# Performance work log

Measured on AMD Instinct MI355X. Metric: run time of the kernel, lower is better.

## Reference

```python
import jax, jax.numpy as jnp
import numpy as np

B, T, D, H = 4, 1024, 1024, 16
DH = D // H
BETA = 0.9


def setup_inputs() -> dict:
    key = jax.random.key(0)
    ks = jax.random.split(key, 9)
    s = 1.0 / np.sqrt(D)
    return {
        "x": jax.random.normal(ks[0], (B, T, D), jnp.float32),
        "l3_memory": jax.random.normal(ks[1], (B, 1, D), jnp.float32),
        "wq": jax.random.normal(ks[2], (D, D), jnp.float32) * s,
        "wk": jax.random.normal(ks[3], (D, D), jnp.float32) * s,
        "wv": jax.random.normal(ks[4], (D, D), jnp.float32) * s,
        "wo": jax.random.normal(ks[5], (D, D), jnp.float32) * s,
        "rw1": jax.random.normal(ks[6], (D, D // 2), jnp.float32) * s,
        "rb1": jnp.zeros((D // 2,), jnp.float32),
        "rw2": jax.random.normal(ks[7], (D // 2, 3), jnp.float32) * (1.0 / np.sqrt(D // 2)),
        "rb2": jnp.zeros((3,), jnp.float32),
    }


def reference(x, l3_memory, wq, wk, wv, wo, rw1, rb1, rw2, rb2):
    b, t, d = x.shape
    dh = d // H

    def heads(y):  # [b,t,d] -> [b,h,t,dh]
        return y.reshape(b, t, H, dh).transpose(0, 2, 1, 3)

    q = x @ wq
    qh = heads(q)

    # L2: causal prefix EMA along time: y_t = beta*y_{t-1} + (1-beta)*x_t, y_{-1}=0
    def ema_step(c, xt):
        y = BETA * c + (1.0 - BETA) * xt
        return y, y
    _, l2 = jax.lax.scan(ema_step, jnp.zeros((b, d), x.dtype), jnp.swapaxes(x, 0, 1))
    l2 = jnp.swapaxes(l2, 0, 1)

    # L3: retrieval memory repeated to sequence length
    l3 = jnp.broadcast_to(l3_memory, (b, t, d))

    mask = jnp.tril(jnp.ones((t, t), bool))
    neg = jnp.finfo(x.dtype).min
    scale = 1.0 / np.sqrt(dh)

    def attend(mem):
        kh = heads(mem @ wk)
        vh = heads(mem @ wv)
        s = jnp.einsum('bhqd,bhkd->bhqk', qh, kh) * scale
        s = jnp.where(mask[None, None], s, neg)
        p = jax.nn.softmax(s, axis=-1)
        return jnp.einsum('bhqk,bhkd->bhqd', p, vh)

    # router over q tokens -> softmax mixture weights [b,t,3]
    hdn = jax.nn.gelu(q @ rw1 + rb1, approximate=False)
    lam = jax.nn.softmax(hdn @ rw2 + rb2, axis=-1)

    mixed = jnp.zeros((b, H, t, dh), x.dtype)
    for i, mem in enumerate((x, l2, l3)):
        mixed = mixed + lam[:, None, :, i:i + 1] * attend(mem)

    out = mixed.transpose(0, 2, 1, 3).reshape(b, t, d) @ wo
    return out, lam
```

## Files before the change

kernel.cpp:

```cpp
#include <hip/hip_runtime.h>
#include <hip/hip_bf16.h>
#include <math.h>


#define B_ 4
#define T_ 1024
#define D_ 1024
#define H_ 16
#define DH_ 64
#define M_ 4096

#define ECH 64
#define NCH 16

typedef __attribute__((ext_vector_type(8))) short bf16x8;
typedef __attribute__((ext_vector_type(4))) short s16x4;
typedef __attribute__((ext_vector_type(4))) float f32x4;

__device__ inline short f2b(float f) {
  __hip_bfloat16 h = __float2bfloat16(f);
  return *reinterpret_cast<short*>(&h);
}

__device__ inline void gload_lds16(const short* g, short* l) {
  __builtin_amdgcn_global_load_lds(
      (const __attribute__((address_space(1))) unsigned int*)g,
      (__attribute__((address_space(3))) unsigned int*)l, 16, 0, 0);
}

__global__ __launch_bounds__(256) void ema_chunk_kernel(const float* __restrict__ x,
                                                        float* __restrict__ l2,
                                                        short* __restrict__ xb) {
  int idx = blockIdx.x * 256 + threadIdx.x;
  int d = idx & (D_ - 1);
  int ch = (idx >> 10) & (NCH - 1);
  int b = idx >> 14;
  const float* xp = x + (size_t)(b * T_ + ch * ECH) * D_ + d;
  float* yp = l2 + (size_t)(b * T_ + ch * ECH) * D_ + d;
  short* xbp = xb + (size_t)(b * T_ + ch * ECH) * D_ + d;
  float y = 0.f;
#pragma unroll 4
  for (int t = 0; t < ECH; ++t) {
    float xv = xp[t * D_];
    y = 0.9f * y + 0.1f * xv;
    yp[t * D_] = y;
    xbp[t * D_] = f2b(xv);
  }
}

__global__ __launch_bounds__(256) void ema_carry_kernel(const float* __restrict__ l2,
                                                        float* __restrict__ g) {
  int idx = blockIdx.x * 256 + threadIdx.x;
  int d = idx & (D_ - 1);
  int b = idx >> 10;
  const float b64 = 0.0011790184577739f;
  float G = 0.f;
  for (int ch = 0; ch < NCH; ++ch) {
    g[(size_t)(b * NCH + ch) * D_ + d] = G;
    float lf = l2[(size_t)(b * T_ + ch * ECH + ECH - 1) * D_ + d];
    G = lf + b64 * G;
  }
}

__global__ __launch_bounds__(256) void ema_fix_kernel(const float* __restrict__ l2,
                                                      const float* __restrict__ g,
                                                      short* __restrict__ l2b) {
  int idx = blockIdx.x * 256 + threadIdx.x;
  int d = idx & (D_ - 1);
  int t = (idx >> 10) & (T_ - 1);
  int b = idx >> 20;
  int ch = t >> 6;
  int off = t & (ECH - 1);
  float G = g[(size_t)(b * NCH + ch) * D_ + d];
  float p9 = exp2f((float)(off + 1) * -0.15200309344504997f);
  l2b[idx] = f2b(l2[idx] + p9 * G);
}

__global__ __launch_bounds__(256) void transpose_w_kernel(
    const float* __restrict__ w0, const float* __restrict__ w1,
    const float* __restrict__ w2, const float* __restrict__ w3,
    const float* __restrict__ w4,
    short* __restrict__ t0, short* __restrict__ t1, short* __restrict__ t2,
    short* __restrict__ t3, short* __restrict__ t4) {
  int z = blockIdx.z;
  const float* W = (z == 0) ? w0 : (z == 1) ? w1 : (z == 2) ? w2 : (z == 3) ? w3 : w4;
  short* Wt = (z == 0) ? t0 : (z == 1) ? t1 : (z == 2) ? t2 : (z == 3) ? t3 : t4;
  int cols = (z == 4) ? 512 : 1024;
  int c0 = blockIdx.x * 32, r0 = blockIdx.y * 32;
  if (c0 >= cols) return;
  __shared__ float tile[32][33];
  int tc = threadIdx.x & 31, tr8 = threadIdx.x >> 5;
#pragma unroll
  for (int i = 0; i < 4; ++i)
    tile[tr8 + i * 8][tc] = W[(size_t)(r0 + tr8 + i * 8) * cols + c0 + tc];
  __syncthreads();
#pragma unroll
  for (int i = 0; i < 4; ++i) {
    int rr = tr8 + i * 8;
    Wt[(size_t)(c0 + rr) * 1024 + r0 + tc] = f2b(tile[tc][rr]);
  }
}

template <int NB>
__global__ __launch_bounds__(256) void gemm_bt(const short* __restrict__ A, int lda,
                                               const short* __restrict__ Bt,
                                               float* __restrict__ Cf,
                                               short* __restrict__ Cb,
                                               int Ndim, int Kdim) {
  __shared__ short As[128 * 64];
  __shared__ short Bs[NB * 64];
  constexpr int NW = NB / 64;
  constexpr int NF = 4;
  constexpr int MF = (NW == 2) ? 4 : 2;
  int tid = threadIdx.x;
  int w = tid >> 6, l = tid & 63;
  int lg = l >> 4, ll = l & 15;
  int wr = (NW == 2) ? (w >> 1) : w;
  int wc = (NW == 2) ? (w & 1) : 0;
  int row0 = blockIdx.y * 128, col0 = blockIdx.x * NB;

  f32x4 acc[MF][NF];
#pragma unroll
  for (int m = 0; m < MF; ++m)
#pragma unroll
    for (int n = 0; n < NF; ++n) acc[m][n] = (f32x4){0.f, 0.f, 0.f, 0.f};

  for (int k0 = 0; k0 < Kdim; k0 += 64) {
    __syncthreads();
#pragma unroll
    for (int it = 0; it < 4; ++it) {
      int s = it * 256 + w * 64 + l;
      int r = s >> 3;
      int c = (s & 7) ^ (r & 7);
      gload_lds16(A + (size_t)(row0 + r) * lda + k0 + c * 8, &As[(it * 256 + w * 64) * 8]);
    }
#pragma unroll
    for (int it = 0; it < NB / 32; ++it) {
      int s = it * 256 + w * 64 + l;
      int r = s >> 3;
      int c = (s & 7) ^ (r & 7);
      gload_lds16(Bt + (size_t)(col0 + r) * Kdim + k0 + c * 8, &Bs[(it * 256 + w * 64) * 8]);
    }
    __syncthreads();
#pragma unroll
    for (int ks = 0; ks < 2; ++ks) {
      bf16x8 af[MF], bfr[NF];
#pragma unroll
      for (int m = 0; m < MF; ++m) {
        int r = wr * (MF * 16) + m * 16 + ll;
        af[m] = *(const bf16x8*)&As[r * 64 + (((ks * 4 + lg) ^ (r & 7)) << 3)];
      }
#pragma unroll
      for (int n = 0; n < NF; ++n) {
        int r = wc * 64 + n * 16 + ll;
        bfr[n] = *(const bf16x8*)&Bs[r * 64 + (((ks * 4 + lg) ^ (r & 7)) << 3)];
      }
#pragma unroll
      for (int m = 0; m < MF; ++m)
#pragma unroll
        for (int n = 0; n < NF; ++n)
          acc[m][n] = __builtin_amdgcn_mfma_f32_16x16x32_bf16(af[m], bfr[n], acc[m][n], 0, 0, 0);
    }
  }
#pragma unroll
  for (int m = 0; m < MF; ++m) {
    int gr = row0 + wr * (MF * 16) + m * 16 + lg * 4;
#pragma unroll
    for (int n = 0; n < NF; ++n) {
      int gc = col0 + wc * 64 + n * 16 + ll;
#pragma unroll
      for (int r = 0; r < 4; ++r) {
        float vv = acc[m][n][r];
        if (Cf) Cf[(size_t)(gr + r) * Ndim + gc] = vv;
        if (Cb) Cb[(size_t)(gr + r) * Ndim + gc] = f2b(vv);
      }
    }
  }
}

__global__ __launch_bounds__(256) void gemm_dual(const short* __restrict__ xb,
                                                 const short* __restrict__ l2b,
                                                 const short* __restrict__ wqkvT,
                                                 short* __restrict__ QKV,
                                                 short* __restrict__ KV2) {
  const short* A;
  const short* Bt;
  short* Cb;
  int Ndim, col0;
  int bx = blockIdx.x;
  if (bx < 24) {
    A = xb; Bt = wqkvT; Cb = QKV; Ndim = 3072; col0 = bx * 128;
  } else {
    A = l2b; Bt = wqkvT + 1024 * 1024; Cb = KV2; Ndim = 2048; col0 = (bx - 24) * 128;
  }
  __shared__ short As[128 * 64];
  __shared__ short Bs[128 * 64];
  int tid = threadIdx.x;
  int w = tid >> 6, l = tid & 63;
  int lg = l >> 4, ll = l & 15;
  int wr = w >> 1, wc = w & 1;
  int row0 = blockIdx.y * 128;

  f32x4 acc[4][4];
#pragma unroll
  for (int m = 0; m < 4; ++m)
#pragma unroll
    for (int n = 0; n < 4; ++n) acc[m][n] = (f32x4){0.f, 0.f, 0.f, 0.f};

  for (int k0 = 0; k0 < 1024; k0 += 64) {
    __syncthreads();
#pragma unroll
    for (int it = 0; it < 4; ++it) {
      int s = it * 256 + w * 64 + l;
      int r = s >> 3;
      int c = (s & 7) ^ (r & 7);
      gload_lds16(A + (size_t)(row0 + r) * 1024 + k0 + c * 8, &As[(it * 256 + w * 64) * 8]);
      gload_lds16(Bt + (size_t)(col0 + r) * 1024 + k0 + c * 8, &Bs[(it * 256 + w * 64) * 8]);
    }
    __syncthreads();
#pragma unroll
    for (int ks = 0; ks < 2; ++ks) {
      bf16x8 af[4], bfr[4];
#pragma unroll
      for (int m = 0; m < 4; ++m) {
        int r = wr * 64 + m * 16 + ll;
        af[m] = *(const bf16x8*)&As[r * 64 + (((ks * 4 + lg) ^ (r & 7)) << 3)];
      }
#pragma unroll
      for (int n = 0; n < 4; ++n) {
        int r = wc * 64 + n * 16 + ll;
        bfr[n] = *(const bf16x8*)&Bs[r * 64 + (((ks * 4 + lg) ^ (r & 7)) << 3)];
      }
#pragma unroll
      for (int m = 0; m < 4; ++m)
#pragma unroll
        for (int n = 0; n < 4; ++n)
          acc[m][n] = __builtin_amdgcn_mfma_f32_16x16x32_bf16(af[m], bfr[n], acc[m][n], 0, 0, 0);
    }
  }
#pragma unroll
  for (int m = 0; m < 4; ++m) {
    int gr = row0 + wr * 64 + m * 16 + lg * 4;
#pragma unroll
    for (int n = 0; n < 4; ++n) {
      int gc = col0 + wc * 64 + n * 16 + ll;
#pragma unroll
      for (int r = 0; r < 4; ++r)
        Cb[(size_t)(gr + r) * Ndim + gc] = f2b(acc[m][n][r]);
    }
  }
}

__global__ __launch_bounds__(256) void v3_kernel(const float* __restrict__ l3,
                                                 const float* __restrict__ wv,
                                                 float* __restrict__ v3) {
  int idx = blockIdx.x * 256 + threadIdx.x;
  int b = idx >> 10;
  int col = idx & 1023;
  const float* xr = l3 + (size_t)b * D_;
  float acc = 0.f;
#pragma unroll 8
  for (int k = 0; k < D_; ++k) acc += xr[k] * wv[(size_t)k * D_ + col];
  v3[idx] = acc;
}

__global__ __launch_bounds__(256) void router_kernel(const float* __restrict__ hdnp,
                                                     const float* __restrict__ rb1,
                                                     const float* __restrict__ rw2,
                                                     const float* __restrict__ rb2,
                                                     float* __restrict__ lam) {
  int wave = (blockIdx.x * 256 + threadIdx.x) >> 6;
  int lane = threadIdx.x & 63;
  const float* hr = hdnp + (size_t)wave * 512;
  float s0 = 0.f, s1 = 0.f, s2 = 0.f;
#pragma unroll
  for (int u = 0; u < 8; ++u) {
    int hcol = u * 64 + lane;
    float vv = hr[hcol] + rb1[hcol];
    float gl = 0.5f * vv * (1.0f + erff(vv * 0.70710678118654752f));
    s0 += gl * rw2[hcol * 3 + 0];
    s1 += gl * rw2[hcol * 3 + 1];
    s2 += gl * rw2[hcol * 3 + 2];
  }
#pragma unroll
  for (int off = 32; off; off >>= 1) {
    s0 += __shfl_xor(s0, off);
    s1 += __shfl_xor(s1, off);
    s2 += __shfl_xor(s2, off);
  }
  if (lane == 0) {
    float a = s0 + rb2[0], bb = s1 + rb2[1], c = s2 + rb2[2];
    float m = fmaxf(fmaxf(a, bb), c);
    float e0 = expf(a - m), e1 = expf(bb - m), e2 = expf(c - m);
    float inv = 1.0f / (e0 + e1 + e2);
    lam[(size_t)wave * 3 + 0] = e0 * inv;
    lam[(size_t)wave * 3 + 1] = e1 * inv;
    lam[(size_t)wave * 3 + 2] = e2 * inv;
  }
}

__global__ __launch_bounds__(256) void attn_fused_kernel(
    const short* __restrict__ q, int ldq,
    const short* __restrict__ k1, const short* __restrict__ v1, int ld1,
    const short* __restrict__ k2, const short* __restrict__ v2, int ld2,
    const float* __restrict__ lam, const float* __restrict__ v3,
    short* __restrict__ mixedb) {
  __shared__ short Ks[2][64][64];
  __shared__ short Vt[2][64][64];
  __shared__ short Ps[4][16][64];

  int bid = blockIdx.x;
  int half = bid >> 9, p = bid & 511;
  int bh = p & 63;
  int j = p >> 6;
  int qb = half ? (15 - j) : j;
  int b = bh >> 4, h = bh & 15;
  int q0 = qb * 64;
  int tid = threadIdx.x;
  int w = tid >> 6, l = tid & 63;
  int lg = l >> 4, ll = l & 15;

  int qw0 = q0 + w * 16;
  bf16x8 qf[2];
  {
    const short* qr = q + (size_t)(b * T_ + qw0 + ll) * ldq + h * DH_;
    qf[0] = *(const bf16x8*)&qr[lg * 8];
    qf[1] = *(const bf16x8*)&qr[32 + lg * 8];
  }

  float m_[2][4];
  f32x4 o[2][4];
  f32x4 ol[2];
#pragma unroll
  for (int s = 0; s < 2; ++s) {
#pragma unroll
    for (int r = 0; r < 4; ++r) m_[s][r] = -1e30f;
#pragma unroll
    for (int db = 0; db < 4; ++db) o[s][db] = (f32x4){0.f, 0.f, 0.f, 0.f};
    ol[s] = (f32x4){0.f, 0.f, 0.f, 0.f};
  }

  bf16x8 ones;
#pragma unroll
  for (int jj = 0; jj < 8; ++jj) ones[jj] = (short)0x3F80;

  const float SC = 0.125f * 1.44269504f;
  int nt = qb + 1;
  for (int t64 = 0; t64 < nt; ++t64) {
    int key0 = t64 * 64;
    __syncthreads();
#pragma unroll
    for (int s = 0; s < 2; ++s) {
      const short* kp = s ? k2 : k1;
      const short* vp = s ? v2 : v1;
      int ld = s ? ld2 : ld1;
#pragma unroll
      for (int it = 0; it < 2; ++it) {
        int e = it * 256 + w * 64 + l;
        int r = e >> 3;
        int cs = (e & 7) ^ (r & 7);
        gload_lds16(kp + (size_t)(b * T_ + key0 + r) * ld + h * DH_ + cs * 8,
                    (short*)Ks[s] + (it * 256 + w * 64) * 8);
      }
      {
        int kp2 = tid >> 3, c8 = tid & 7;
        size_t gi = (size_t)(b * T_ + key0 + kp2 * 2) * ld + h * DH_ + c8 * 8;
        bf16x8 va = *(const bf16x8*)&vp[gi];
        bf16x8 vb = *(const bf16x8*)&vp[gi + ld];
        unsigned int* Vtd = (unsigned int*)Vt[s];
#pragma unroll
        for (int jj = 0; jj < 8; ++jj) {
          int dh = c8 * 8 + jj;
          int X = ((dh ^ (dh >> 3)) & 7) << 2;
          Vtd[dh * 32 + (kp2 ^ X)] =
              ((unsigned int)(unsigned short)va[jj]) |
              (((unsigned int)(unsigned short)vb[jj]) << 16);
        }
      }
    }
    __syncthreads();
    if (key0 > qw0 + 15) continue;

#pragma unroll
    for (int s = 0; s < 2; ++s) {
      f32x4 c[4];
#pragma unroll
      for (int kt = 0; kt < 4; ++kt) c[kt] = (f32x4){0.f, 0.f, 0.f, 0.f};
      __builtin_amdgcn_s_setprio(1);
#pragma unroll
      for (int kt = 0; kt < 4; ++kt) {
        int kr = kt * 16 + ll;
        bf16x8 kfa = *(const bf16x8*)&Ks[s][kr][((lg ^ (kr & 7)) << 3)];
        bf16x8 kfb = *(const bf16x8*)&Ks[s][kr][(((4 + lg) ^ (kr & 7)) << 3)];
        c[kt] = __builtin_amdgcn_mfma_f32_16x16x32_bf16(qf[0], kfa, c[kt], 0, 0, 0);
        c[kt] = __builtin_amdgcn_mfma_f32_16x16x32_bf16(qf[1], kfb, c[kt], 0, 0, 0);
      }
      __builtin_amdgcn_s_setprio(0);

      float sv[4][4];
      if (key0 + 63 <= qw0) {
#pragma unroll
        for (int r = 0; r < 4; ++r)
#pragma unroll
          for (int kt = 0; kt < 4; ++kt) sv[r][kt] = c[kt][r] * SC;
      } else {
#pragma unroll
        for (int r = 0; r < 4; ++r) {
          int grow = qw0 + lg * 4 + r;
#pragma unroll
          for (int kt = 0; kt < 4; ++kt) {
            float t = c[kt][r] * SC;
            sv[r][kt] = (key0 + kt * 16 + ll > grow) ? -1e30f : t;
          }
        }
      }

      float mx[4];
#pragma unroll
      for (int r = 0; r < 4; ++r) {
        float m0 = fmaxf(fmaxf(sv[r][0], sv[r][1]), fmaxf(sv[r][2], sv[r][3]));
        m0 = fmaxf(m0, __shfl_xor(m0, 1));
        m0 = fmaxf(m0, __shfl_xor(m0, 2));
        m0 = fmaxf(m0, __shfl_xor(m0, 4));
        m0 = fmaxf(m0, __shfl_xor(m0, 8));
        mx[r] = m0;
      }
      int grew = 0;
#pragma unroll
      for (int r = 0; r < 4; ++r) grew |= (mx[r] > m_[s][r] + 8.f) ? 1 : 0;
      if (__any(grew)) {
#pragma unroll
        for (int r = 0; r < 4; ++r) {
          float nm = fmaxf(m_[s][r], mx[r]);
          float al = exp2f(m_[s][r] - nm);
          m_[s][r] = nm;
          ol[s][r] *= al;
#pragma unroll
          for (int db = 0; db < 4; ++db) o[s][db][r] *= al;
        }
      }

#pragma unroll
      for (int r = 0; r < 4; ++r) {
        float mr = m_[s][r];
        int prow = lg * 4 + r;
#pragma unroll
        for (int kt = 0; kt < 4; ++kt) {
          float pv = exp2f(sv[r][kt] - mr);
          Ps[w][prow][((kt ^ lg) << 4) + ll] = f2b(pv);
        }
      }
      asm volatile("s_waitcnt lgkmcnt(0)" ::: "memory");
      __builtin_amdgcn_sched_barrier(0);

      __builtin_amdgcn_s_setprio(1);
#pragma unroll
      for (int ks = 0; ks < 2; ++ks) {
        int pswz = (ks * 32 + lg * 8) ^ ((ll >> 2) << 4);
        bf16x8 pf = *(const bf16x8*)&Ps[w][ll][pswz];
        const unsigned int* Vtd = (const unsigned int*)Vt[s];
        ol[s] = __builtin_amdgcn_mfma_f32_16x16x32_bf16(pf, ones, ol[s], 0, 0, 0);
#pragma unroll
        for (int db = 0; db < 4; ++db) {
          int dh = db * 16 + ll;
          int X = ((dh ^ (dh >> 3)) & 7) << 2;
          bf16x8 vf = *(const bf16x8*)&Vtd[dh * 32 + ((ks * 16 + lg * 4) ^ X)];
          o[s][db] = __builtin_amdgcn_mfma_f32_16x16x32_bf16(pf, vf, o[s][db], 0, 0, 0);
        }
      }
      __builtin_amdgcn_s_setprio(0);
      __builtin_amdgcn_sched_barrier(0);
    }
  }

#pragma unroll
  for (int r = 0; r < 4; ++r) {
    int grow = qw0 + lg * 4 + r;
    const float* lr = lam + (size_t)(b * T_ + grow) * 3;
    float w0 = lr[0] / ol[0][r];
    float w1 = lr[1] / ol[1][r];
    float w2 = lr[2];
#pragma unroll
    for (int db = 0; db < 4; ++db) {
      int dcol = h * DH_ + db * 16 + ll;
      float val = w0 * o[0][db][r] + w1 * o[1][db][r] + w2 * v3[(b << 10) + dcol];
      mixedb[(size_t)(b * T_ + grow) * D_ + dcol] = f2b(val);
    }
  }
}

extern "C" void kernel_launch(void* const* d_in, const int* in_sizes, int n_in,
                              void* d_out, int out_size, void* d_ws, size_t ws_size,
                              hipStream_t stream) {
  const float* x = (const float*)d_in[0];
  const float* l3m = (const float*)d_in[1];
  const float* wq = (const float*)d_in[2];
  const float* wk = (const float*)d_in[3];
  const float* wv = (const float*)d_in[4];
  const float* wo = (const float*)d_in[5];
  const float* rw1 = (const float*)d_in[6];
  const float* rb1 = (const float*)d_in[7];
  const float* rw2 = (const float*)d_in[8];
  const float* rb2 = (const float*)d_in[9];

  float* out = (float*)d_out;
  float* lam = out + (size_t)M_ * D_;

  float* ws = (float*)d_ws;
  float* l2 = ws;
  short* QKV = (short*)ws;
  float* hdnp = ws + 6291456;
  float* v3 = ws + 8388608;
  float* gbuf = ws + 8392704;
  short* sb = (short*)(ws + 8458240);
  short* xb = sb;
  short* l2b = sb + 4194304;
  short* KV2 = sb + 8388608;
  short* mixedb = sb + 16777216;
  short* wqkvT = sb + 20971520;
  short* woT = sb + 24117248;
  short* rw1T = sb + 25165824;

  dim3 blk(256);

  transpose_w_kernel<<<dim3(32, 32, 5), blk, 0, stream>>>(
      wq, wk, wv, wo, rw1,
      wqkvT, wqkvT + 1024 * 1024, wqkvT + 2048 * 1024, woT, rw1T);

  ema_chunk_kernel<<<256, blk, 0, stream>>>(x, l2, xb);
  ema_carry_kernel<<<16, blk, 0, stream>>>(l2, gbuf);
  ema_fix_kernel<<<16384, blk, 0, stream>>>(l2, gbuf, l2b);

  gemm_dual<<<dim3(40, 32), blk, 0, stream>>>(xb, l2b, wqkvT, QKV, KV2);

  gemm_bt<64><<<dim3(8, 32), blk, 0, stream>>>(QKV, 3072, rw1T, hdnp, (short*)nullptr, 512, 1024);
  router_kernel<<<1024, blk, 0, stream>>>(hdnp, rb1, rw2, rb2, lam);

  v3_kernel<<<16, blk, 0, stream>>>(l3m, wv, v3);

  attn_fused_kernel<<<1024, blk, 0, stream>>>(QKV, 3072,
                                              QKV + 1024, QKV + 2048, 3072,
                                              KV2, KV2 + 1024, 2048,
                                              lam, v3, mixedb);

  gemm_bt<64><<<dim3(16, 32), blk, 0, stream>>>(mixedb, 1024, woT, out, (short*)nullptr, 1024, 1024);
}
```

Before: 252.0 us.

## Transpose attention MFMA layout to keep P in registers via shuffles

The attention kernel swaps MFMA operand order so each lane owns one query row. Row max becomes a per-lane reduction plus two shuffles, and the P tile is packed to bf16 and redistributed with lane shuffles instead of a round trip through LDS. Output stores are vectorized to 4-wide bf16. The GEMM remaps block indices for L2-friendly grouping, and the attention grid reverses causal block ordering so heavy blocks start first. In exchange it adds many shuffle instructions and changes the scheduling assumptions.

```diff
diff --git a/kernel.cpp b/kernel.cpp
--- a/kernel.cpp
+++ b/kernel.cpp
@@ -16,10 +16,16 @@
 typedef __attribute__((ext_vector_type(8))) short bf16x8;
 typedef __attribute__((ext_vector_type(4))) short s16x4;
 typedef __attribute__((ext_vector_type(4))) float f32x4;
+typedef __attribute__((ext_vector_type(4))) unsigned int u32x4;
 
 __device__ inline short f2b(float f) {
   __hip_bfloat16 h = __float2bfloat16(f);
   return *reinterpret_cast<short*>(&h);
+}
+
+__device__ inline unsigned int pack2(float lo, float hi) {
+  return ((unsigned int)(unsigned short)f2b(hi) << 16) |
+         (unsigned int)(unsigned short)f2b(lo);
 }
 
 __device__ inline void gload_lds16(const short* g, short* l) {
@@ -183,11 +189,15 @@
                                                  const short* __restrict__ wqkvT,
                                                  short* __restrict__ QKV,
                                                  short* __restrict__ KV2) {
+  int lin = blockIdx.y * 40 + blockIdx.x;
+  int lin2 = (lin & 7) * 160 + (lin >> 3);
+  int bx = lin2 % 40;
+  int by = lin2 / 40;
+
   const short* A;
   const short* Bt;
   short* Cb;
   int Ndim, col0;
-  int bx = blockIdx.x;
   if (bx < 24) {
     A = xb; Bt = wqkvT; Cb = QKV; Ndim = 3072; col0 = bx * 128;
   } else {
@@ -199,7 +209,7 @@
   int w = tid >> 6, l = tid & 63;
   int lg = l >> 4, ll = l & 15;
   int wr = w >> 1, wc = w & 1;
-  int row0 = blockIdx.y * 128;
+  int row0 = by * 128;
 
   f32x4 acc[4][4];
 #pragma unroll
@@ -307,13 +317,12 @@
     short* __restrict__ mixedb) {
   __shared__ short Ks[2][64][64];
   __shared__ short Vt[2][64][64];
-  __shared__ short Ps[4][16][64];
 
   int bid = blockIdx.x;
   int half = bid >> 9, p = bid & 511;
   int bh = p & 63;
   int j = p >> 6;
-  int qb = half ? (15 - j) : j;
+  int qb = half ? j : (15 - j);
   int b = bh >> 4, h = bh & 15;
   int q0 = qb * 64;
   int tid = threadIdx.x;
@@ -328,13 +337,12 @@
     qf[1] = *(const bf16x8*)&qr[32 + lg * 8];
   }
 
-  float m_[2][4];
+  float m_[2];
   f32x4 o[2][4];
   f32x4 ol[2];
 #pragma unroll
   for (int s = 0; s < 2; ++s) {
-#pragma unroll
-    for (int r = 0; r < 4; ++r) m_[s][r] = -1e30f;
+    m_[s] = -1e30f;
 #pragma unroll
     for (int db = 0; db < 4; ++db) o[s][db] = (f32x4){0.f, 0.f, 0.f, 0.f};
     ol[s] = (f32x4){0.f, 0.f, 0.f, 0.f};
@@ -343,6 +351,10 @@
   bf16x8 ones;
 #pragma unroll
   for (int jj = 0; jj < 8; ++jj) ones[jj] = (short)0x3F80;
+
+  int se = ll + (((2 * lg) & 3) << 4);
+  int so = ll + (((2 * lg + 1) & 3) << 4);
+  bool hi = (lg >= 2);
 
   const float SC = 0.125f * 1.44269504f;
   int nt = qb + 1;
@@ -392,100 +404,92 @@
         int kr = kt * 16 + ll;
         bf16x8 kfa = *(const bf16x8*)&Ks[s][kr][((lg ^ (kr & 7)) << 3)];
         bf16x8 kfb = *(const bf16x8*)&Ks[s][kr][(((4 + lg) ^ (kr & 7)) << 3)];
-        c[kt] = __builtin_amdgcn_mfma_f32_16x16x32_bf16(qf[0], kfa, c[kt], 0, 0, 0);
-        c[kt] = __builtin_amdgcn_mfma_f32_16x16x32_bf16(qf[1], kfb, c[kt], 0, 0, 0);
+        c[kt] = __builtin_amdgcn_mfma_f32_16x16x32_bf16(kfa, qf[0], c[kt], 0, 0, 0);
+        c[kt] = __builtin_amdgcn_mfma_f32_16x16x32_bf16(kfb, qf[1], c[kt], 0, 0, 0);
       }
       __builtin_amdgcn_s_setprio(0);
 
-      float sv[4][4];
+      float sv[16];
+      int row = qw0 + ll;
       if (key0 + 63 <= qw0) {
 #pragma unroll
-        for (int r = 0; r < 4; ++r)
-#pragma unroll
-          for (int kt = 0; kt < 4; ++kt) sv[r][kt] = c[kt][r] * SC;
+        for (int kt = 0; kt < 4; ++kt)
+#pragma unroll
+          for (int r = 0; r < 4; ++r) sv[kt * 4 + r] = c[kt][r] * SC;
       } else {
 #pragma unroll
-        for (int r = 0; r < 4; ++r) {
-          int grow = qw0 + lg * 4 + r;
-#pragma unroll
-          for (int kt = 0; kt < 4; ++kt) {
+        for (int kt = 0; kt < 4; ++kt)
+#pragma unroll
+          for (int r = 0; r < 4; ++r) {
             float t = c[kt][r] * SC;
-            sv[r][kt] = (key0 + kt * 16 + ll > grow) ? -1e30f : t;
+            sv[kt * 4 + r] = (key0 + kt * 16 + lg * 4 + r > row) ? -1e30f : t;
           }
-        }
-      }
-
-      float mx[4];
-#pragma unroll
-      for (int r = 0; r < 4; ++r) {
-        float m0 = fmaxf(fmaxf(sv[r][0], sv[r][1]), fmaxf(sv[r][2], sv[r][3]));
-        m0 = fmaxf(m0, __shfl_xor(m0, 1));
-        m0 = fmaxf(m0, __shfl_xor(m0, 2));
-        m0 = fmaxf(m0, __shfl_xor(m0, 4));
-        m0 = fmaxf(m0, __shfl_xor(m0, 8));
-        mx[r] = m0;
-      }
-      int grew = 0;
-#pragma unroll
-      for (int r = 0; r < 4; ++r) grew |= (mx[r] > m_[s][r] + 8.f) ? 1 : 0;
-      if (__any(grew)) {
-#pragma unroll
-        for (int r = 0; r < 4; ++r) {
-          float nm = fmaxf(m_[s][r], mx[r]);
-          float al = exp2f(m_[s][r] - nm);
-          m_[s][r] = nm;
-          ol[s][r] *= al;
-#pragma unroll
-          for (int db = 0; db < 4; ++db) o[s][db][r] *= al;
-        }
-      }
-
-#pragma unroll
-      for (int r = 0; r < 4; ++r) {
-        float mr = m_[s][r];
-        int prow = lg * 4 + r;
-#pragma unroll
-        for (int kt = 0; kt < 4; ++kt) {
-          float pv = exp2f(sv[r][kt] - mr);
-          Ps[w][prow][((kt ^ lg) << 4) + ll] = f2b(pv);
-        }
-      }
-      asm volatile("s_waitcnt lgkmcnt(0)" ::: "memory");
-      __builtin_amdgcn_sched_barrier(0);
-
-      __builtin_amdgcn_s_setprio(1);
+      }
+
+      float mx = sv[0];
+#pragma unroll
+      for (int i = 1; i < 16; ++i) mx = fmaxf(mx, sv[i]);
+      mx = fmaxf(mx, __shfl_xor(mx, 16));
+      mx = fmaxf(mx, __shfl_xor(mx, 32));
+
+      if (__any(mx > m_[s] + 8.f)) {
+        float nm = fmaxf(m_[s], mx);
+        float al = exp2f(m_[s] - nm);
+        m_[s] = nm;
+        ol[s] *= al;
+#pragma unroll
+        for (int db = 0; db < 4; ++db) o[s][db] *= al;
+      }
+
+      unsigned int pk[4][2];
+#pragma unroll
+      for (int kt = 0; kt < 4; ++kt) {
+        float p0 = exp2f(sv[kt * 4 + 0] - m_[s]);
+        float p1 = exp2f(sv[kt * 4 + 1] - m_[s]);
+        float p2 = exp2f(sv[kt * 4 + 2] - m_[s]);
+        float p3 = exp2f(sv[kt * 4 + 3] - m_[s]);
+        pk[kt][0] = pack2(p0, p1);
+        pk[kt][1] = pack2(p2, p3);
+      }
+
+      const unsigned int* Vtd = (const unsigned int*)Vt[s];
 #pragma unroll
       for (int ks = 0; ks < 2; ++ks) {
-        int pswz = (ks * 32 + lg * 8) ^ ((ll >> 2) << 4);
-        bf16x8 pf = *(const bf16x8*)&Ps[w][ll][pswz];
-        const unsigned int* Vtd = (const unsigned int*)Vt[s];
-        ol[s] = __builtin_amdgcn_mfma_f32_16x16x32_bf16(pf, ones, ol[s], 0, 0, 0);
+        unsigned int a0 = __shfl(pk[2 * ks][0], se), b0 = __shfl(pk[2 * ks + 1][0], se);
+        unsigned int a1 = __shfl(pk[2 * ks][1], se), b1 = __shfl(pk[2 * ks + 1][1], se);
+        unsigned int a2 = __shfl(pk[2 * ks][0], so), b2 = __shfl(pk[2 * ks + 1][0], so);
+        unsigned int a3 = __shfl(pk[2 * ks][1], so), b3 = __shfl(pk[2 * ks + 1][1], so);
+        u32x4 pd = {hi ? b0 : a0, hi ? b1 : a1, hi ? b2 : a2, hi ? b3 : a3};
+        bf16x8 pf = *(bf16x8*)&pd;
+        __builtin_amdgcn_s_setprio(1);
+        ol[s] = __builtin_amdgcn_mfma_f32_16x16x32_bf16(ones, pf, ol[s], 0, 0, 0);
 #pragma unroll
         for (int db = 0; db < 4; ++db) {
           int dh = db * 16 + ll;
           int X = ((dh ^ (dh >> 3)) & 7) << 2;
           bf16x8 vf = *(const bf16x8*)&Vtd[dh * 32 + ((ks * 16 + lg * 4) ^ X)];
-          o[s][db] = __builtin_amdgcn_mfma_f32_16x16x32_bf16(pf, vf, o[s][db], 0, 0, 0);
+          o[s][db] = __builtin_amdgcn_mfma_f32_16x16x32_bf16(vf, pf, o[s][db], 0, 0, 0);
         }
-      }
-      __builtin_amdgcn_s_setprio(0);
-      __builtin_amdgcn_sched_barrier(0);
-    }
-  }
-
-#pragma unroll
-  for (int r = 0; r < 4; ++r) {
-    int grow = qw0 + lg * 4 + r;
-    const float* lr = lam + (size_t)(b * T_ + grow) * 3;
-    float w0 = lr[0] / ol[0][r];
-    float w1 = lr[1] / ol[1][r];
-    float w2 = lr[2];
-#pragma unroll
-    for (int db = 0; db < 4; ++db) {
-      int dcol = h * DH_ + db * 16 + ll;
+        __builtin_amdgcn_s_setprio(0);
+      }
+    }
+  }
+
+  int grow = qw0 + ll;
+  const float* lr = lam + (size_t)(b * T_ + grow) * 3;
+  float w0 = lr[0] / ol[0][0];
+  float w1 = lr[1] / ol[1][0];
+  float w2 = lr[2];
+#pragma unroll
+  for (int db = 0; db < 4; ++db) {
+    s16x4 pkv;
+#pragma unroll
+    for (int r = 0; r < 4; ++r) {
+      int dcol = h * DH_ + db * 16 + lg * 4 + r;
       float val = w0 * o[0][db][r] + w1 * o[1][db][r] + w2 * v3[(b << 10) + dcol];
-      mixedb[(size_t)(b * T_ + grow) * D_ + dcol] = f2b(val);
-    }
+      pkv[r] = f2b(val);
+    }
+    *(s16x4*)&mixedb[(size_t)(b * T_ + grow) * D_ + h * DH_ + db * 16 + lg * 4] = pkv;
   }
 }
 
```

Result: slower. 258.4 us (+2.5%).
